# Optimization experiments

Measured on AMD Instinct MI355X. Metric: run time of the kernel, lower is better.

## Reference

```python
import jax, jax.numpy as jnp
import numpy as np
import math

D_MODEL = 512; NHEAD = 8; D_FF = 2048
DS_HEADS = 4; DS_DEPTH = 156; EPS = 1e-5
B = 128; N = 300; M = 300


def _ln(x, g, b):
    m = x.mean(-1, keepdims=True)
    v = ((x - m) ** 2).mean(-1, keepdims=True)
    return (x - m) / jnp.sqrt(v + EPS) * g + b


def _mish(x):
    return x * jnp.tanh(jax.nn.softplus(x))


def _mha(xq, xk, xv, in_w, in_b, out_w, out_b, nhead):
    D = xq.shape[-1]; dh = D // nhead
    wq, wk, wv = jnp.split(in_w, 3, axis=0)
    bq, bk, bv = jnp.split(in_b, 3)
    def proj(x, w, b):
        y = x @ w.T + b
        Bm, Nn, _ = y.shape
        return y.reshape(Bm, Nn, nhead, dh).transpose(0, 2, 1, 3)
    q, k, v = proj(xq, wq, bq), proj(xk, wk, bk), proj(xv, wv, bv)
    s = jnp.einsum('bhqd,bhkd->bhqk', q, k) / math.sqrt(dh)
    p = jax.nn.softmax(s, axis=-1)
    o = jnp.einsum('bhqk,bhkd->bhqd', p, v)
    Bm, _, Nn, _ = o.shape
    o = o.transpose(0, 2, 1, 3).reshape(Bm, Nn, D)
    return o @ out_w.T + out_b


def _custom_weight(p):
    # sequential kinematic-tree averaging on the post-softmax [...,24,24] matrix
    def upd(p, i, j, si, sj):
        return p.at[..., i, j].set((p[..., i, j] + p[..., si, sj]) * 0.5)
    p = upd(p, 0, 6, 0, 3); p = upd(p, 6, 0, 3, 0)
    p = upd(p, 0, 9, 0, 6); p = upd(p, 9, 0, 6, 0)
    for idx in (12, 13, 14):
        p = upd(p, 0, idx, 0, 9); p = upd(p, idx, 0, 9, 0)
    for s, tgt in ((13, 16), (14, 17), (12, 15)):
        p = upd(p, 0, tgt, 0, s); p = upd(p, tgt, 0, s, 0)
    return p


def _ds_attn(x, qk_w, v_w, lw, lb):
    Bm, Nn, _ = x.shape
    comb = jnp.einsum('bnf,fx->bnx', x, qk_w)
    q, k = jnp.split(comb, 2, axis=2)
    v = jnp.einsum('bnf,fx->bnx', x, v_w)
    def heads(y):
        return y.reshape(Bm, Nn, DS_HEADS, DS_DEPTH).transpose(0, 2, 1, 3)
    q, k, v = heads(q), heads(k), heads(v)  # [B,H,N,156]
    qs = q[..., 3:147].reshape(Bm, DS_HEADS, Nn, 24, 6)
    ks = k[..., 3:147].reshape(Bm, DS_HEADS, Nn, 24, 6)
    vs = v[..., 3:147].reshape(Bm, DS_HEADS, Nn, 24, 6)
    s = jnp.einsum('bhnij,bhnkj->bhnik', qs, ks) / math.sqrt(6.0)
    p = _custom_weight(jax.nn.softmax(s, axis=-1))
    o = jnp.einsum('bhnik,bhnkj->bhnij', p, vs).reshape(Bm, DS_HEADS, Nn, 144)
    v = v.at[..., 3:147].set(o)
    v = v.transpose(0, 2, 1, 3).reshape(Bm, Nn, DS_HEADS * DS_DEPTH)
    return v @ lw.T + lb


def _align(x_d, t, w, b):
    tt = t + x_d.mean(axis=-2)           # [B,D]
    h = _mish(tt) @ w.T + b              # [B,2D]
    weight, bias = jnp.split(h, 2, axis=-1)
    return (weight[:, None, :] + 1.0) * x_d + bias[:, None, :]


def _forward(tgt, memory, t, qk_w, v_w, ds_lw, ds_lb,
             ta_in_w, ta_in_b, ta_out_w, ta_out_b,
             ca_in_w, ca_in_b, ca_out_w, ca_out_b,
             l1_w, l1_b, l2_w, l2_b,
             n1_g, n1_b, n2_g, n2_b, n3_g, n3_b, n4_g, n4_b,
             a1_w, a1_b, a2_w, a2_b, a3_w, a3_b):
    x = tgt
    x = x + _ds_attn(_ln(x, n1_g, n1_b), qk_w, v_w, ds_lw, ds_lb)
    xn = _ln(x, n2_g, n2_b)
    x2 = _mha(xn, xn, xn, ta_in_w, ta_in_b, ta_out_w, ta_out_b, NHEAD)
    x = x + _align(x2, t, a1_w, a1_b)
    x3 = _mha(_ln(x, n3_g, n3_b), memory, memory, ca_in_w, ca_in_b, ca_out_w, ca_out_b, NHEAD)
    x = x + _align(x3, t, a2_w, a2_b)
    xn4 = _ln(x, n4_g, n4_b)
    x4 = jax.nn.relu(xn4 @ l1_w.T + l1_b) @ l2_w.T + l2_b
    x = x + _align(x4, t, a3_w, a3_b)
    return x


def setup_inputs():
    key = jax.random.key(0)
    ks = iter(jax.random.split(key, 64))
    def nrm(shape, s=0.02):
        return jax.random.normal(next(ks), shape, dtype=jnp.float32) * s
    z = lambda *shape: jnp.zeros(shape, jnp.float32)
    o = lambda *shape: jnp.ones(shape, jnp.float32)
    D = D_MODEL
    inp = {
        'tgt': jax.random.normal(next(ks), (B, N, D), dtype=jnp.float32),
        'memory': jax.random.normal(next(ks), (B, M, D), dtype=jnp.float32),
        't': jax.random.normal(next(ks), (B, D), dtype=jnp.float32),
        'qk_w': nrm((D, 2 * DS_DEPTH * DS_HEADS)),
        'v_w': nrm((D, DS_DEPTH * DS_HEADS)),
        'ds_lw': nrm((D, DS_DEPTH * DS_HEADS)), 'ds_lb': z(D),
        'ta_in_w': nrm((3 * D, D)), 'ta_in_b': z(3 * D),
        'ta_out_w': nrm((D, D)), 'ta_out_b': z(D),
        'ca_in_w': nrm((3 * D, D)), 'ca_in_b': z(3 * D),
        'ca_out_w': nrm((D, D)), 'ca_out_b': z(D),
        'l1_w': nrm((D_FF, D)), 'l1_b': z(D_FF),
        'l2_w': nrm((D, D_FF)), 'l2_b': z(D),
        'n1_g': o(D), 'n1_b': z(D), 'n2_g': o(D), 'n2_b': z(D),
        'n3_g': o(D), 'n3_b': z(D), 'n4_g': o(D), 'n4_b': z(D),
        'a1_w': nrm((2 * D, D)), 'a1_b': z(2 * D),
        'a2_w': nrm((2 * D, D)), 'a2_b': z(2 * D),
        'a3_w': nrm((2 * D, D)), 'a3_b': z(2 * D),
        'cond_drop_prob': 0,
    }
    return inp


def reference(tgt, memory, t, qk_w, v_w, ds_lw, ds_lb,
              ta_in_w, ta_in_b, ta_out_w, ta_out_b,
              ca_in_w, ca_in_b, ca_out_w, ca_out_b,
              l1_w, l1_b, l2_w, l2_b,
              n1_g, n1_b, n2_g, n2_b, n3_g, n3_b, n4_g, n4_b,
              a1_w, a1_b, a2_w, a2_b, a3_w, a3_b, cond_drop_prob):
    # cond_drop_prob is unused in the torch forward body (dropout eval mode)
    return _forward(tgt, memory, t, qk_w, v_w, ds_lw, ds_lb,
                    ta_in_w, ta_in_b, ta_out_w, ta_out_b,
                    ca_in_w, ca_in_b, ca_out_w, ca_out_b,
                    l1_w, l1_b, l2_w, l2_b,
                    n1_g, n1_b, n2_g, n2_b, n3_g, n3_b, n4_g, n4_b,
                    a1_w, a1_b, a2_w, a2_b, a3_w, a3_b)
```

## Files before the change

### kernel.cpp

```cpp
#include <hip/hip_runtime.h>
#include <math.h>

#define DEV __device__ __forceinline__

static constexpr int BB   = 128;
static constexpr int NN   = 300;
static constexpr int DM   = 512;

typedef __attribute__((ext_vector_type(8))) short short8;
typedef __attribute__((ext_vector_type(4))) float f32x4;

DEV unsigned short f2bf(float f) {
  unsigned u = __float_as_uint(f);
  unsigned r = (u + 0x7fffu + ((u >> 16) & 1u)) >> 16;
  return (unsigned short)r;
}
DEV float bf2f(unsigned short s) { return __uint_as_float((unsigned)s << 16); }
DEV unsigned pack_bf16x2(float a, float b) {
  return (unsigned)f2bf(a) | ((unsigned)f2bf(b) << 16);
}
DEV unsigned pack_trunc(float a, float b) {
  return (__float_as_uint(a) >> 16) | (__float_as_uint(b) & 0xffff0000u);
}

DEV void gld16(const void* g, void* l) {
  __builtin_amdgcn_global_load_lds(
      (const __attribute__((address_space(1))) unsigned int*)g,
      (__attribute__((address_space(3))) unsigned int*)l,
      16, 0, 0);
}

__global__ __launch_bounds__(256) void ln_kernel(
    const float* __restrict__ X, const float* __restrict__ g,
    const float* __restrict__ b, unsigned short* __restrict__ Y, int rows)
{
  int wv = threadIdx.x >> 6, lane = threadIdx.x & 63;
  int row = blockIdx.x * 4 + wv;
  if (row >= rows) return;
  const float* xp = X + (size_t)row * DM;
  float v[8]; float s = 0.f, s2 = 0.f;
#pragma unroll
  for (int j = 0; j < 8; j++) {
    v[j] = xp[lane + 64 * j]; s += v[j]; s2 += v[j] * v[j];
  }
#pragma unroll
  for (int o = 32; o >= 1; o >>= 1) { s += __shfl_xor(s, o); s2 += __shfl_xor(s2, o); }
  float mean = s * (1.f / 512.f);
  float var  = s2 * (1.f / 512.f) - mean * mean;
  float rstd = rsqrtf(var + 1e-5f);
  unsigned short* yp = Y + (size_t)row * DM;
#pragma unroll
  for (int j = 0; j < 8; j++) {
    int c = lane + 64 * j;
    yp[c] = f2bf((v[j] - mean) * rstd * g[c] + b[c]);
  }
}

__global__ __launch_bounds__(256) void align_ln(
    float* __restrict__ X, const float* __restrict__ Y,
    const float* __restrict__ H,
    const float* __restrict__ g, const float* __restrict__ bb,
    unsigned short* __restrict__ XN)
{
  int wv = threadIdx.x >> 6, lane = threadIdx.x & 63;
  int row = blockIdx.x * 4 + wv;
  int b = row / NN;
  float* xp = X + (size_t)row * DM;
  const float* yp = Y + (size_t)row * DM;
  const float* hw = H + (size_t)b * 1024;
  const float* hb = hw + 512;
  float v[8]; float s = 0.f, s2 = 0.f;
#pragma unroll
  for (int j = 0; j < 8; j++) {
    int c = lane + 64 * j;
    float xv = xp[c] + (hw[c] + 1.f) * yp[c] + hb[c];
    v[j] = xv; s += xv; s2 += xv * xv;
  }
#pragma unroll
  for (int j = 0; j < 8; j++) xp[lane + 64 * j] = v[j];
#pragma unroll
  for (int o = 32; o >= 1; o >>= 1) { s += __shfl_xor(s, o); s2 += __shfl_xor(s2, o); }
  float mean = s * (1.f / 512.f);
  float var  = s2 * (1.f / 512.f) - mean * mean;
  float rstd = rsqrtf(var + 1e-5f);
  unsigned short* yn = XN + (size_t)row * DM;
#pragma unroll
  for (int j = 0; j < 8; j++) {
    int c = lane + 64 * j;
    yn[c] = f2bf((v[j] - mean) * rstd * g[c] + bb[c]);
  }
}

__global__ __launch_bounds__(256) void cvt_bf16(
    const float* __restrict__ in, unsigned short* __restrict__ out, int n4)
{
  int i = blockIdx.x * 256 + threadIdx.x;
  if (i >= n4) return;
  float4 v = ((const float4*)in)[i];
  union { unsigned short s[4]; uint2 u; } o;
  o.s[0] = f2bf(v.x); o.s[1] = f2bf(v.y); o.s[2] = f2bf(v.z); o.s[3] = f2bf(v.w);
  *(uint2*)&out[(size_t)i * 4] = o.u;
}

__global__ __launch_bounds__(256) void cvt_pad_bf16(
    const float* __restrict__ in, unsigned short* __restrict__ out,
    int R, int C, int Cpad)
{
  int idx = blockIdx.x * 256 + threadIdx.x;
  int r = idx / Cpad, c = idx % Cpad;
  if (r >= R) return;
  out[idx] = (c < C) ? f2bf(in[(size_t)r * C + c]) : (unsigned short)0;
}

__global__ __launch_bounds__(256) void transpose_bf16(
    const float* __restrict__ in, unsigned short* __restrict__ out,
    int R, int Ccols, int Cpad)
{
  __shared__ float t[32][33];
  int c0 = blockIdx.x * 32, r0 = blockIdx.y * 32;
  int x = threadIdx.x & 31, y = threadIdx.x >> 5;
#pragma unroll
  for (int dy = 0; dy < 32; dy += 8) {
    int r = r0 + y + dy, c = c0 + x;
    t[y + dy][x] = (r < R && c < Ccols) ? in[(size_t)r * Ccols + c] : 0.f;
  }
  __syncthreads();
#pragma unroll
  for (int dy = 0; dy < 32; dy += 8) {
    int c = c0 + y + dy, r = r0 + x;
    if (c < Cpad && r < R) out[(size_t)c * R + r] = f2bf(t[x][y + dy]);
  }
}

template<int EPI>
__global__ __launch_bounds__(256) void gemm_bb(
    const unsigned short* __restrict__ A, int lda,
    const unsigned short* __restrict__ W, int ldw,
    const float* __restrict__ bias,
    const float* __restrict__ R, int ldr,
    void* __restrict__ Cv, int ldc,
    int M, int K, int NC)
{
  __shared__ __align__(16) unsigned short As[128 * 32];
  __shared__ __align__(16) unsigned short Bs[128 * 32];
  const int tid = threadIdx.x;
  const int wave = tid >> 6, lane = tid & 63;
  const int wr = wave >> 1, wc = wave & 1;
  const int quad = lane >> 4, l16 = lane & 15;

  const unsigned nx = gridDim.x, nwg = nx * gridDim.y;
  const unsigned orig = blockIdx.y * nx + blockIdx.x;
  const unsigned qq = nwg >> 3, rr = nwg & 7;
  const unsigned xcd = orig & 7, idx = orig >> 3;
  const unsigned swz = (xcd < rr) ? (xcd * (qq + 1) + idx)
                                  : (rr * (qq + 1) + (xcd - rr) * qq + idx);
  const int n0 = (int)(swz % nx) * 128;
  const int m0 = (int)(swz / nx) * 128;

  int ra = m0 + (tid >> 2);
  int ra0 = (ra      >= M) ? M - 1 : ra;
  int ra1 = (ra + 64 >= M) ? M - 1 : ra + 64;
  const unsigned short* a0 = A + (size_t)ra0 * lda + (tid & 3) * 8;
  const unsigned short* a1 = A + (size_t)ra1 * lda + (tid & 3) * 8;
  const unsigned short* b0 = W + (size_t)(n0 + (tid >> 2)) * ldw + (tid & 3) * 8;
  const unsigned short* b1 = b0 + (size_t)64 * ldw;
  unsigned short* dA0 = &As[wave * 512];
  unsigned short* dA1 = &As[2048 + wave * 512];
  unsigned short* dB0 = &Bs[wave * 512];
  unsigned short* dB1 = &Bs[2048 + wave * 512];

  f32x4 acc[4][4];
#pragma unroll
  for (int i = 0; i < 4; i++)
#pragma unroll
    for (int j = 0; j < 4; j++) acc[i][j] = (f32x4){0.f, 0.f, 0.f, 0.f};

  for (int k0 = 0; k0 < K; k0 += 32) {
    gld16(a0 + k0, dA0);
    gld16(a1 + k0, dA1);
    gld16(b0 + k0, dB0);
    gld16(b1 + k0, dB1);
    __syncthreads();
    short8 af[4], bq[4];
#pragma unroll
    for (int i = 0; i < 4; i++)
      af[i] = *(const short8*)&As[(wr * 64 + i * 16 + l16) * 32 + quad * 8];
#pragma unroll
    for (int j = 0; j < 4; j++)
      bq[j] = *(const short8*)&Bs[(wc * 64 + j * 16 + l16) * 32 + quad * 8];
#pragma unroll
    for (int i = 0; i < 4; i++)
#pragma unroll
      for (int j = 0; j < 4; j++)
        acc[i][j] = __builtin_amdgcn_mfma_f32_16x16x32_bf16(af[i], bq[j], acc[i][j], 0, 0, 0);
    __syncthreads();
  }

#pragma unroll
  for (int i = 0; i < 4; i++) {
    int rbase = m0 + wr * 64 + i * 16 + quad * 4;
#pragma unroll
    for (int r = 0; r < 4; r++) {
      int row = rbase + r;
      if (row < M) {
        size_t rowc = (size_t)row * ldc;
#pragma unroll
        for (int j = 0; j < 4; j++) {
          int col = n0 + wc * 64 + j * 16 + l16;
          if (col < NC) {
            float e = acc[i][j][r];
            if (EPI == 1 || EPI == 2 || EPI == 3 || EPI == 5) e += bias[col];
            if (EPI == 3) e += R[(size_t)row * ldr + col];
            if (EPI == 2) {
              ((unsigned short*)Cv)[rowc + col] = f2bf(fmaxf(e, 0.f));
            } else if (EPI == 5 || EPI == 6) {
              ((unsigned short*)Cv)[rowc + col] = f2bf(e);
            } else {
              ((float*)Cv)[rowc + col] = e;
            }
          }
        }
      }
    }
  }
}

__global__ __launch_bounds__(256) void ds_attn_kernel(
    const float* __restrict__ COMB, unsigned short* __restrict__ V)
{
  __shared__ float ks[4][2][24][6];
  __shared__ float vs[4][2][24][6];
  int wv = threadIdx.x >> 6, lane = threadIdx.x & 63;
  int half = lane >> 5, i = lane & 31;
  int u  = blockIdx.x * 4 + wv;
  int bn = u >> 1, hp = u & 1;
  int h  = hp * 2 + half;
  size_t cbase = (size_t)bn * 1248 + h * 156 + 3;
  size_t vbase = (size_t)bn * 640  + h * 156 + 3;

  float q[6];
  if (i < 24) {
#pragma unroll
    for (int j = 0; j < 6; j++) {
      q[j]                 = COMB[cbase + i * 6 + j];
      ks[wv][half][i][j]   = COMB[cbase + 624 + i * 6 + j];
      vs[wv][half][i][j]   = bf2f(V[vbase + i * 6 + j]);
    }
  } else {
#pragma unroll
    for (int j = 0; j < 6; j++) q[j] = 0.f;
  }
  __syncthreads();

  float p[24];
#pragma unroll
  for (int k = 0; k < 24; k++) p[k] = 0.f;

  if (i < 24) {
    float mx = -1e30f;
#pragma unroll
    for (int k = 0; k < 24; k++) {
      float s = 0.f;
#pragma unroll
      for (int j = 0; j < 6; j++) s += q[j] * ks[wv][half][k][j];
      s *= 0.4082482904638631f;
      p[k] = s; mx = fmaxf(mx, s);
    }
    float sum = 0.f;
#pragma unroll
    for (int k = 0; k < 24; k++) { p[k] = __expf(p[k] - mx); sum += p[k]; }
    float inv = 1.f / sum;
#pragma unroll
    for (int k = 0; k < 24; k++) p[k] *= inv;
  }

  {
    float c = p[0];
    float t;
    t = __shfl(c, 3, 32);  if (i == 6) c = (c + t) * 0.5f;
    t = __shfl(c, 6, 32);  if (i == 9) c = (c + t) * 0.5f;
    t = __shfl(c, 9, 32);  if (i >= 12 && i <= 14) c = (c + t) * 0.5f;
    int src = (i >= 3) ? (i - 3) : 0;
    t = __shfl(c, src, 32); if (i >= 15 && i <= 17) c = (c + t) * 0.5f;
    p[0] = c;
  }
  if (i == 0) {
    p[6]  = (p[6]  + p[3])  * 0.5f;
    p[9]  = (p[9]  + p[6])  * 0.5f;
    p[12] = (p[12] + p[9])  * 0.5f;
    p[13] = (p[13] + p[9])  * 0.5f;
    p[14] = (p[14] + p[9])  * 0.5f;
    p[16] = (p[16] + p[13]) * 0.5f;
    p[17] = (p[17] + p[14]) * 0.5f;
    p[15] = (p[15] + p[12]) * 0.5f;
  }

  if (i < 24) {
    float o[6] = {0.f, 0.f, 0.f, 0.f, 0.f, 0.f};
#pragma unroll
    for (int k = 0; k < 24; k++) {
#pragma unroll
      for (int j = 0; j < 6; j++) o[j] += p[k] * vs[wv][half][k][j];
    }
#pragma unroll
    for (int j = 0; j < 6; j++) V[vbase + i * 6 + j] = f2bf(o[j]);
  }
}

__global__ __launch_bounds__(512) void mha_mfma(
    const unsigned short* __restrict__ Qp, int ldq, int qoff,
    const unsigned short* __restrict__ KVp, int ldkv, int koff, int voff,
    unsigned short* __restrict__ Op, float scale)
{
  __shared__ __align__(16) unsigned short Ksh[304 * 72];
  __shared__ __align__(16) unsigned short Qsh[304 * 72];
  __shared__ __align__(16) unsigned short Vt[64 * 328];
  __shared__ __align__(16) unsigned short Pt[8][16 * 68];
  const int bh = blockIdx.x, b = bh >> 3, h = bh & 7;
  const int tid = threadIdx.x, wv = tid >> 6, lane = tid & 63;
  const int quad = lane >> 4, l16 = lane & 15;
  const size_t kbase = (size_t)b * NN * ldkv + koff + h * 64;
  const size_t vbase = (size_t)b * NN * ldkv + voff + h * 64;
  const size_t qbase = (size_t)b * NN * ldq  + qoff + h * 64;

  for (int f = tid; f < 304 * 8; f += 512) {
    int rk = f >> 3, c8 = (f & 7) * 8;
    short8 wk, wq;
    if (rk < 300) {
      wk = *(const short8*)(KVp + kbase + (size_t)rk * ldkv + c8);
      wq = *(const short8*)(Qp  + qbase + (size_t)rk * ldq  + c8);
    } else {
      union { uint4 u; short8 s; } z; z.u = make_uint4(0u, 0u, 0u, 0u);
      wk = z.s; wq = z.s;
    }
    *(short8*)&Ksh[rk * 72 + c8] = wk;
    *(short8*)&Qsh[rk * 72 + c8] = wq;
  }
  for (int f = tid; f < 64 * 164; f += 512) {
    int d = f & 63, s0 = (f >> 6) * 2;
    unsigned w = 0u;
    if (s0 < 300) {
      unsigned short v0 = KVp[vbase + (size_t)s0 * ldkv + d];
      unsigned short v1 = (s0 + 1 < 300) ? KVp[vbase + (size_t)(s0 + 1) * ldkv + d]
                                         : (unsigned short)0;
      w = (unsigned)v0 | ((unsigned)v1 << 16);
    }
    *(unsigned*)&Vt[d * 328 + s0] = w;
  }
  __syncthreads();

  unsigned short* pt = &Pt[wv][0];

  for (int qt = wv; qt < 19; qt += 8) {
    int qr = qt * 16 + l16;
    short8 qf[2];
    qf[0] = *(const short8*)&Qsh[qr * 72 + quad * 8];
    qf[1] = *(const short8*)&Qsh[qr * 72 + 32 + quad * 8];

    f32x4 sacc[19];
#pragma unroll
    for (int t = 0; t < 19; t++) {
      short8 k0 = *(const short8*)&Ksh[(t * 16 + l16) * 72 + quad * 8];
      short8 k1 = *(const short8*)&Ksh[(t * 16 + l16) * 72 + 32 + quad * 8];
      f32x4 a = (f32x4){0.f, 0.f, 0.f, 0.f};
      a = __builtin_amdgcn_mfma_f32_16x16x32_bf16(k0, qf[0], a, 0, 0, 0);
      a = __builtin_amdgcn_mfma_f32_16x16x32_bf16(k1, qf[1], a, 0, 0, 0);
      sacc[t] = a;
    }

    float mx = -1e30f;
#pragma unroll
    for (int t = 0; t < 19; t++)
#pragma unroll
      for (int r = 0; r < 4; r++) mx = fmaxf(mx, sacc[t][r]);
    mx = fmaxf(mx, __shfl_xor(mx, 16));
    mx = fmaxf(mx, __shfl_xor(mx, 32));
    float sum = 0.f;
#pragma unroll
    for (int t = 0; t < 19; t++) {
#pragma unroll
      for (int r = 0; r < 4; r++) {
        float p = __expf((sacc[t][r] - mx) * scale);
        if (t == 18 && quad == 3) p = 0.f;
        sacc[t][r] = p; sum += p;
      }
    }
    sum += __shfl_xor(sum, 16);
    sum += __shfl_xor(sum, 32);
    float inv = 1.f / sum;

    f32x4 oacc[4];
#pragma unroll
    for (int dt = 0; dt < 4; dt++) oacc[dt] = (f32x4){0.f, 0.f, 0.f, 0.f};
#pragma unroll
    for (int c = 0; c < 10; c++) {
#pragma unroll
      for (int tic = 0; tic < 2; tic++) {
        int t = 2 * c + tic;
        unsigned w0 = 0u, w1 = 0u;
        if (t < 19) {
          w0 = pack_trunc(sacc[t][0], sacc[t][1]);
          w1 = pack_trunc(sacc[t][2], sacc[t][3]);
        }
        *(unsigned*)&pt[l16 * 68 + tic * 16 + quad * 4]     = w0;
        *(unsigned*)&pt[l16 * 68 + tic * 16 + quad * 4 + 2] = w1;
      }
      short8 pa = *(const short8*)&pt[l16 * 68 + quad * 8];
#pragma unroll
      for (int dt = 0; dt < 4; dt++) {
        short8 vb = *(const short8*)&Vt[(dt * 16 + l16) * 328 + c * 32 + quad * 8];
        oacc[dt] = __builtin_amdgcn_mfma_f32_16x16x32_bf16(pa, vb, oacc[dt], 0, 0, 0);
      }
    }

#pragma unroll
    for (int r = 0; r < 4; r++) {
      float iv = __shfl(inv, quad * 4 + r);
#pragma unroll
      for (int dt = 0; dt < 4; dt++)
        pt[(quad * 4 + r) * 68 + dt * 16 + l16] = f2bf(oacc[dt][r] * iv);
    }
#pragma unroll
    for (int rep = 0; rep < 2; rep++) {
      int idx = rep * 64 + lane;
      int rl = idx >> 3, seg = idx & 7;
      int row = qt * 16 + rl;
      uint4 w = *(const uint4*)&pt[rl * 68 + seg * 8];
      if (row < 300)
        *(uint4*)(Op + (size_t)(b * NN + row) * DM + h * 64 + seg * 8) = w;
    }
  }
}

__global__ __launch_bounds__(256) void colmean_mish(
    const float* __restrict__ Y, const float* __restrict__ tvec,
    unsigned short* __restrict__ mm)
{
  int g = blockIdx.x * 256 + threadIdx.x;
  int b = g >> 9, d = g & 511;
  const float* yp = Y + (size_t)b * NN * DM + d;
  float s = 0.f;
  for (int n = 0; n < NN; n++) s += yp[(size_t)n * DM];
  float v = tvec[g] + s * (1.f / 300.f);
  float sp = (v > 20.f) ? v : log1pf(__expf(v));
  mm[g] = f2bf(v * tanhf(sp));
}

__global__ __launch_bounds__(256) void align_apply(
    float* __restrict__ X, const float* __restrict__ Y,
    const float* __restrict__ H)
{
  int idx = blockIdx.x * 256 + threadIdx.x;
  int row = idx >> 7;
  int d4  = (idx & 127) * 4;
  int b   = row / NN;
  float4 y = *(const float4*)&Y[(size_t)row * DM + d4];
  float4 x = *(const float4*)&X[(size_t)row * DM + d4];
  const float* hw = H + (size_t)b * 1024 + d4;
  const float* hb = hw + 512;
  x.x += (hw[0] + 1.f) * y.x + hb[0];
  x.y += (hw[1] + 1.f) * y.y + hb[1];
  x.z += (hw[2] + 1.f) * y.z + hb[2];
  x.w += (hw[3] + 1.f) * y.w + hb[3];
  *(float4*)&X[(size_t)row * DM + d4] = x;
}

extern "C" void kernel_launch(void* const* d_in, const int* in_sizes, int n_in,
                              void* d_out, int out_size, void* d_ws, size_t ws_size,
                              hipStream_t stream)
{
  const float* tgt      = (const float*)d_in[0];
  const float* memory   = (const float*)d_in[1];
  const float* tvec     = (const float*)d_in[2];
  const float* qk_w     = (const float*)d_in[3];
  const float* v_w      = (const float*)d_in[4];
  const float* ds_lw    = (const float*)d_in[5];
  const float* ds_lb    = (const float*)d_in[6];
  const float* ta_in_w  = (const float*)d_in[7];
  const float* ta_in_b  = (const float*)d_in[8];
  const float* ta_out_w = (const float*)d_in[9];
  const float* ta_out_b = (const float*)d_in[10];
  const float* ca_in_w  = (const float*)d_in[11];
  const float* ca_in_b  = (const float*)d_in[12];
  const float* ca_out_w = (const float*)d_in[13];
  const float* ca_out_b = (const float*)d_in[14];
  const float* l1_w     = (const float*)d_in[15];
  const float* l1_b     = (const float*)d_in[16];
  const float* l2_w     = (const float*)d_in[17];
  const float* l2_b     = (const float*)d_in[18];
  const float* n1_g = (const float*)d_in[19]; const float* n1_b = (const float*)d_in[20];
  const float* n2_g = (const float*)d_in[21]; const float* n2_b = (const float*)d_in[22];
  const float* n3_g = (const float*)d_in[23]; const float* n3_b = (const float*)d_in[24];
  const float* n4_g = (const float*)d_in[25]; const float* n4_b = (const float*)d_in[26];
  const float* a1_w = (const float*)d_in[27]; const float* a1_b = (const float*)d_in[28];
  const float* a2_w = (const float*)d_in[29]; const float* a2_b = (const float*)d_in[30];
  const float* a3_w = (const float*)d_in[31]; const float* a3_b = (const float*)d_in[32];

  const size_t W_QKT = 1280ULL * 512 * 2;
  const size_t W_VT  = 640ULL  * 512 * 2;
  const size_t W_TAI = 1536ULL * 512 * 2;
  const size_t W_TAO = 512ULL  * 512 * 2;
  const size_t W_CAI = 1536ULL * 512 * 2;
  const size_t W_CAO = 512ULL  * 512 * 2;
  const size_t W_L1  = 2048ULL * 512 * 2;
  const size_t W_L2  = 512ULL  * 2048 * 2;
  const size_t W_DSL = 512ULL  * 640 * 2;
  const size_t W_AX  = 1024ULL * 512 * 2;
  const size_t W_MEM = (size_t)BB * NN * 512 * 2;
  const size_t fixedB = W_QKT + W_VT + W_TAI + W_TAO + W_CAI + W_CAO
                      + W_L1 + W_L2 + W_DSL + 3 * W_AX + W_MEM;
  const size_t per_b = 300ULL * (1024 + 4992 + 1280 + 2048) + 1024 + 4096;
  int Bc = 128;
  while (Bc > 16 && fixedB + (size_t)Bc * per_b > ws_size) Bc >>= 1;
  const int rows = Bc * NN;
  const int mB   = (rows + 127) / 128;
  const int aB   = (Bc + 127) / 128;
  const int nchunks = BB / Bc;

  char* p = (char*)d_ws;
  unsigned short* qkTh  = (unsigned short*)p; p += W_QKT;
  unsigned short* vTh   = (unsigned short*)p; p += W_VT;
  unsigned short* taiWh = (unsigned short*)p; p += W_TAI;
  unsigned short* taoWh = (unsigned short*)p; p += W_TAO;
  unsigned short* caiWh = (unsigned short*)p; p += W_CAI;
  unsigned short* caoWh = (unsigned short*)p; p += W_CAO;
  unsigned short* l1Wh  = (unsigned short*)p; p += W_L1;
  unsigned short* l2Wh  = (unsigned short*)p; p += W_L2;
  unsigned short* dslWh = (unsigned short*)p; p += W_DSL;
  unsigned short* a1Wh  = (unsigned short*)p; p += W_AX;
  unsigned short* a2Wh  = (unsigned short*)p; p += W_AX;
  unsigned short* a3Wh  = (unsigned short*)p; p += W_AX;
  unsigned short* memh  = (unsigned short*)p; p += W_MEM;
  unsigned short* XNh   = (unsigned short*)p; p += (size_t)rows * 512 * 2;
  char* SCRB = p;                             p += (size_t)rows * 4992;
  unsigned short* Vdsh  = (unsigned short*)p; p += (size_t)rows * 640 * 2;
  float* Yb  = (float*)p; p += (size_t)rows * 512 * 4;
  unsigned short* MMh = (unsigned short*)p;   p += (size_t)Bc * 512 * 2;
  float* Hb  = (float*)p;

  float* COMB = (float*)SCRB;
  unsigned short* QKVh = (unsigned short*)SCRB;
  unsigned short* T2h  = (unsigned short*)SCRB;

  dim3 thr(256);

  transpose_bf16<<<dim3(40, 16), thr, 0, stream>>>(qk_w, qkTh, 512, 1248, 1280);
  transpose_bf16<<<dim3(20, 16), thr, 0, stream>>>(v_w,  vTh,  512, 624, 640);
  cvt_pad_bf16<<<dim3(512 * 640 / 256), thr, 0, stream>>>(ds_lw, dslWh, 512, 624, 640);
  auto cvt = [&](const float* src, unsigned short* dst, size_t n) {
    int n4 = (int)(n / 4);
    cvt_bf16<<<dim3((n4 + 255) / 256), thr, 0, stream>>>(src, dst, n4);
  };
  cvt(ta_in_w,  taiWh, 1536ULL * 512);
  cvt(ta_out_w, taoWh, 512ULL * 512);
  cvt(ca_in_w,  caiWh, 1536ULL * 512);
  cvt(ca_out_w, caoWh, 512ULL * 512);
  cvt(l1_w,     l1Wh,  2048ULL * 512);
  cvt(l2_w,     l2Wh,  512ULL * 2048);
  cvt(a1_w,     a1Wh,  1024ULL * 512);
  cvt(a2_w,     a2Wh,  1024ULL * 512);
  cvt(a3_w,     a3Wh,  1024ULL * 512);
  cvt(memory,   memh,  (size_t)BB * NN * 512);

  for (int c = 0; c < nchunks; ++c) {
    const size_t roff = (size_t)c * Bc * NN * DM;
    const float* tgtC = tgt    + roff;
    const float* tC   = tvec   + (size_t)c * Bc * 512;
    const unsigned short* memhC = memh + roff;
    float*       XC   = (float*)d_out + roff;

    ln_kernel<<<rows / 4, thr, 0, stream>>>(tgtC, n1_g, n1_b, XNh, rows);
    gemm_bb<0><<<dim3(10, mB), thr, 0, stream>>>(XNh, 512, qkTh, 512, nullptr, nullptr, 0, COMB, 1248, rows, 512, 1248);
    gemm_bb<6><<<dim3(5, mB),  thr, 0, stream>>>(XNh, 512, vTh,  512, nullptr, nullptr, 0, Vdsh, 640,  rows, 512, 640);
    ds_attn_kernel<<<rows / 2, thr, 0, stream>>>(COMB, Vdsh);
    gemm_bb<3><<<dim3(4, mB),  thr, 0, stream>>>(Vdsh, 640, dslWh, 640, ds_lb, tgtC, 512, XC, 512, rows, 640, 512);

    ln_kernel<<<rows / 4, thr, 0, stream>>>(XC, n2_g, n2_b, XNh, rows);
    gemm_bb<5><<<dim3(12, mB), thr, 0, stream>>>(XNh, 512, taiWh, 512, ta_in_b, nullptr, 0, QKVh, 1536, rows, 512, 1536);
    mha_mfma<<<Bc * 8, 512, 0, stream>>>(QKVh, 1536, 0, QKVh, 1536, 512, 1024, XNh, 0.125f);
    gemm_bb<1><<<dim3(4, mB),  thr, 0, stream>>>(XNh, 512, taoWh, 512, ta_out_b, nullptr, 0, Yb, 512, rows, 512, 512);
    colmean_mish<<<Bc * 2, thr, 0, stream>>>(Yb, tC, MMh);
    gemm_bb<1><<<dim3(8, aB),  thr, 0, stream>>>(MMh, 512, a1Wh, 512, a1_b, nullptr, 0, Hb, 1024, Bc, 512, 1024);
    align_ln<<<rows / 4, thr, 0, stream>>>(XC, Yb, Hb, n3_g, n3_b, XNh);

    gemm_bb<5><<<dim3(4, mB),  thr, 0, stream>>>(XNh, 512, caiWh, 512, ca_in_b, nullptr, 0, QKVh, 1536, rows, 512, 512);
    gemm_bb<5><<<dim3(8, mB),  thr, 0, stream>>>(memhC, 512, caiWh + 512 * 512, 512, ca_in_b + 512, nullptr, 0, QKVh + 512, 1536, rows, 512, 1024);
    mha_mfma<<<Bc * 8, 512, 0, stream>>>(QKVh, 1536, 0, QKVh, 1536, 512, 1024, XNh, 0.125f);
    gemm_bb<1><<<dim3(4, mB),  thr, 0, stream>>>(XNh, 512, caoWh, 512, ca_out_b, nullptr, 0, Yb, 512, rows, 512, 512);
    colmean_mish<<<Bc * 2, thr, 0, stream>>>(Yb, tC, MMh);
    gemm_bb<1><<<dim3(8, aB),  thr, 0, stream>>>(MMh, 512, a2Wh, 512, a2_b, nullptr, 0, Hb, 1024, Bc, 512, 1024);
    align_ln<<<rows / 4, thr, 0, stream>>>(XC, Yb, Hb, n4_g, n4_b, XNh);

    gemm_bb<2><<<dim3(16, mB), thr, 0, stream>>>(XNh, 512, l1Wh, 512, l1_b, nullptr, 0, T2h, 2048, rows, 512, 2048);
    gemm_bb<1><<<dim3(4, mB),  thr, 0, stream>>>(T2h, 2048, l2Wh, 2048, l2_b, nullptr, 0, Yb, 512, rows, 2048, 512);
    colmean_mish<<<Bc * 2, thr, 0, stream>>>(Yb, tC, MMh);
    gemm_bb<1><<<dim3(8, aB),  thr, 0, stream>>>(MMh, 512, a3Wh, 512, a3_b, nullptr, 0, Hb, 1024, Bc, 512, 1024);
    align_apply<<<rows / 2, thr, 0, stream>>>(XC, Yb, Hb);
  }
}
```

Baseline: 2.295 ms.

## Write QKV in head-major layout, fuse DS qk/v GEMMs, store COMB as bf16

The QKV projection GEMMs now scatter their output into a head-major [sec][head][row][64] bf16 layout. mha_mfma can then load K, V and Q contiguously, and it reads Q fragments straight from global memory instead of staging them in shared memory. The depth-split qk and v projections are merged into one GEMM over a concatenated weight, and the COMB intermediate is stored in bf16 instead of fp32, which shrinks scratch and memory traffic. The trade-offs are scattered epilogue stores, lower precision on q/k, and uncoalesced global Q reads.

```diff
diff --git a/kernel.cpp b/kernel.cpp
--- a/kernel.cpp
+++ b/kernel.cpp
@@ -16,9 +16,6 @@
   return (unsigned short)r;
 }
 DEV float bf2f(unsigned short s) { return __uint_as_float((unsigned)s << 16); }
-DEV unsigned pack_bf16x2(float a, float b) {
-  return (unsigned)f2bf(a) | ((unsigned)f2bf(b) << 16);
-}
 DEV unsigned pack_trunc(float a, float b) {
   return (__float_as_uint(a) >> 16) | (__float_as_uint(b) & 0xffff0000u);
 }
@@ -139,7 +136,7 @@
     const float* __restrict__ bias,
     const float* __restrict__ R, int ldr,
     void* __restrict__ Cv, int ldc,
-    int M, int K, int NC)
+    int M, int K, int NC, int coloff)
 {
   __shared__ __align__(16) unsigned short As[128 * 32];
   __shared__ __align__(16) unsigned short Bs[128 * 32];
@@ -209,12 +206,19 @@
           int col = n0 + wc * 64 + j * 16 + l16;
           if (col < NC) {
             float e = acc[i][j][r];
-            if (EPI == 1 || EPI == 2 || EPI == 3 || EPI == 5) e += bias[col];
+            if (EPI == 1 || EPI == 2 || EPI == 3 || EPI == 7) e += bias[col];
             if (EPI == 3) e += R[(size_t)row * ldr + col];
             if (EPI == 2) {
               ((unsigned short*)Cv)[rowc + col] = f2bf(fmaxf(e, 0.f));
-            } else if (EPI == 5 || EPI == 6) {
-              ((unsigned short*)Cv)[rowc + col] = f2bf(e);
+            } else if (EPI == 7) {
+              int cc = col + coloff;
+              int sec = cc >> 9, hh = (cc >> 6) & 7, dh = cc & 63;
+              ((unsigned short*)Cv)[(((size_t)(sec * 8 + hh)) * M + row) * 64 + dh] = f2bf(e);
+            } else if (EPI == 8) {
+              if (col < 1248)
+                ((unsigned short*)Cv)[(size_t)row * 1248 + col] = f2bf(e);
+              else if (col >= 1280)
+                ((unsigned short*)(void*)R)[(size_t)row * 640 + (col - 1280)] = f2bf(e);
             } else {
               ((float*)Cv)[rowc + col] = e;
             }
@@ -226,7 +230,7 @@
 }
 
 __global__ __launch_bounds__(256) void ds_attn_kernel(
-    const float* __restrict__ COMB, unsigned short* __restrict__ V)
+    const unsigned short* __restrict__ COMB, unsigned short* __restrict__ V)
 {
   __shared__ float ks[4][2][24][6];
   __shared__ float vs[4][2][24][6];
@@ -242,8 +246,8 @@
   if (i < 24) {
 #pragma unroll
     for (int j = 0; j < 6; j++) {
-      q[j]                 = COMB[cbase + i * 6 + j];
-      ks[wv][half][i][j]   = COMB[cbase + 624 + i * 6 + j];
+      q[j]                 = bf2f(COMB[cbase + i * 6 + j]);
+      ks[wv][half][i][j]   = bf2f(COMB[cbase + 624 + i * 6 + j]);
       vs[wv][half][i][j]   = bf2f(V[vbase + i * 6 + j]);
     }
   } else {
@@ -308,41 +312,35 @@
 }
 
 __global__ __launch_bounds__(512) void mha_mfma(
-    const unsigned short* __restrict__ Qp, int ldq, int qoff,
-    const unsigned short* __restrict__ KVp, int ldkv, int koff, int voff,
-    unsigned short* __restrict__ Op, float scale)
+    const unsigned short* __restrict__ QKV3, unsigned short* __restrict__ Op,
+    int rowsT, float scale)
 {
   __shared__ __align__(16) unsigned short Ksh[304 * 72];
-  __shared__ __align__(16) unsigned short Qsh[304 * 72];
   __shared__ __align__(16) unsigned short Vt[64 * 328];
   __shared__ __align__(16) unsigned short Pt[8][16 * 68];
   const int bh = blockIdx.x, b = bh >> 3, h = bh & 7;
   const int tid = threadIdx.x, wv = tid >> 6, lane = tid & 63;
   const int quad = lane >> 4, l16 = lane & 15;
-  const size_t kbase = (size_t)b * NN * ldkv + koff + h * 64;
-  const size_t vbase = (size_t)b * NN * ldkv + voff + h * 64;
-  const size_t qbase = (size_t)b * NN * ldq  + qoff + h * 64;
+  const unsigned short* Qp = QKV3 + ((size_t)h        * rowsT + b * NN) * 64;
+  const unsigned short* Kp = QKV3 + ((size_t)(8 + h)  * rowsT + b * NN) * 64;
+  const unsigned short* Vp = QKV3 + ((size_t)(16 + h) * rowsT + b * NN) * 64;
 
   for (int f = tid; f < 304 * 8; f += 512) {
     int rk = f >> 3, c8 = (f & 7) * 8;
-    short8 wk, wq;
+    short8 w;
     if (rk < 300) {
-      wk = *(const short8*)(KVp + kbase + (size_t)rk * ldkv + c8);
-      wq = *(const short8*)(Qp  + qbase + (size_t)rk * ldq  + c8);
+      w = *(const short8*)(Kp + f * 8);
     } else {
-      union { uint4 u; short8 s; } z; z.u = make_uint4(0u, 0u, 0u, 0u);
-      wk = z.s; wq = z.s;
-    }
-    *(short8*)&Ksh[rk * 72 + c8] = wk;
-    *(short8*)&Qsh[rk * 72 + c8] = wq;
+      union { uint4 u; short8 s; } z; z.u = make_uint4(0u, 0u, 0u, 0u); w = z.s;
+    }
+    *(short8*)&Ksh[rk * 72 + c8] = w;
   }
   for (int f = tid; f < 64 * 164; f += 512) {
     int d = f & 63, s0 = (f >> 6) * 2;
     unsigned w = 0u;
     if (s0 < 300) {
-      unsigned short v0 = KVp[vbase + (size_t)s0 * ldkv + d];
-      unsigned short v1 = (s0 + 1 < 300) ? KVp[vbase + (size_t)(s0 + 1) * ldkv + d]
-                                         : (unsigned short)0;
+      unsigned short v0 = Vp[s0 * 64 + d];
+      unsigned short v1 = (s0 + 1 < 300) ? Vp[(s0 + 1) * 64 + d] : (unsigned short)0;
       w = (unsigned)v0 | ((unsigned)v1 << 16);
     }
     *(unsigned*)&Vt[d * 328 + s0] = w;
@@ -352,10 +350,10 @@
   unsigned short* pt = &Pt[wv][0];
 
   for (int qt = wv; qt < 19; qt += 8) {
-    int qr = qt * 16 + l16;
+    int qr = qt * 16 + l16; if (qr > 299) qr = 299;
     short8 qf[2];
-    qf[0] = *(const short8*)&Qsh[qr * 72 + quad * 8];
-    qf[1] = *(const short8*)&Qsh[qr * 72 + 32 + quad * 8];
+    qf[0] = *(const short8*)(Qp + qr * 64 + quad * 8);
+    qf[1] = *(const short8*)(Qp + qr * 64 + 32 + quad * 8);
 
     f32x4 sacc[19];
 #pragma unroll
@@ -496,8 +494,7 @@
   const float* a2_w = (const float*)d_in[29]; const float* a2_b = (const float*)d_in[30];
   const float* a3_w = (const float*)d_in[31]; const float* a3_b = (const float*)d_in[32];
 
-  const size_t W_QKT = 1280ULL * 512 * 2;
-  const size_t W_VT  = 640ULL  * 512 * 2;
+  const size_t W_W2  = 1920ULL * 512 * 2;
   const size_t W_TAI = 1536ULL * 512 * 2;
   const size_t W_TAO = 512ULL  * 512 * 2;
   const size_t W_CAI = 1536ULL * 512 * 2;
@@ -507,9 +504,9 @@
   const size_t W_DSL = 512ULL  * 640 * 2;
   const size_t W_AX  = 1024ULL * 512 * 2;
   const size_t W_MEM = (size_t)BB * NN * 512 * 2;
-  const size_t fixedB = W_QKT + W_VT + W_TAI + W_TAO + W_CAI + W_CAO
+  const size_t fixedB = W_W2 + W_TAI + W_TAO + W_CAI + W_CAO
                       + W_L1 + W_L2 + W_DSL + 3 * W_AX + W_MEM;
-  const size_t per_b = 300ULL * (1024 + 4992 + 1280 + 2048) + 1024 + 4096;
+  const size_t per_b = 300ULL * (1024 + 4096 + 1280 + 2048) + 1024 + 4096;
   int Bc = 128;
   while (Bc > 16 && fixedB + (size_t)Bc * per_b > ws_size) Bc >>= 1;
   const int rows = Bc * NN;
@@ -518,8 +515,7 @@
   const int nchunks = BB / Bc;
 
   char* p = (char*)d_ws;
-  unsigned short* qkTh  = (unsigned short*)p; p += W_QKT;
-  unsigned short* vTh   = (unsigned short*)p; p += W_VT;
+  unsigned short* W2h   = (unsigned short*)p; p += W_W2;
   unsigned short* taiWh = (unsigned short*)p; p += W_TAI;
   unsigned short* taoWh = (unsigned short*)p; p += W_TAO;
   unsigned short* caiWh = (unsigned short*)p; p += W_CAI;
@@ -532,20 +528,20 @@
   unsigned short* a3Wh  = (unsigned short*)p; p += W_AX;
   unsigned short* memh  = (unsigned short*)p; p += W_MEM;
   unsigned short* XNh   = (unsigned short*)p; p += (size_t)rows * 512 * 2;
-  char* SCRB = p;                             p += (size_t)rows * 4992;
+  char* SCRB = p;                             p += (size_t)rows * 4096;
   unsigned short* Vdsh  = (unsigned short*)p; p += (size_t)rows * 640 * 2;
   float* Yb  = (float*)p; p += (size_t)rows * 512 * 4;
   unsigned short* MMh = (unsigned short*)p;   p += (size_t)Bc * 512 * 2;
   float* Hb  = (float*)p;
 
-  float* COMB = (float*)SCRB;
-  unsigned short* QKVh = (unsigned short*)SCRB;
-  unsigned short* T2h  = (unsigned short*)SCRB;
+  unsigned short* COMBh = (unsigned short*)SCRB;
+  unsigned short* QKV3  = (unsigned short*)SCRB;
+  unsigned short* T2h   = (unsigned short*)SCRB;
 
   dim3 thr(256);
 
-  transpose_bf16<<<dim3(40, 16), thr, 0, stream>>>(qk_w, qkTh, 512, 1248, 1280);
-  transpose_bf16<<<dim3(20, 16), thr, 0, stream>>>(v_w,  vTh,  512, 624, 640);
+  transpose_bf16<<<dim3(40, 16), thr, 0, stream>>>(qk_w, W2h, 512, 1248, 1280);
+  transpose_bf16<<<dim3(20, 16), thr, 0, stream>>>(v_w,  W2h + 1280 * 512, 512, 624, 640);
   cvt_pad_bf16<<<dim3(512 * 640 / 256), thr, 0, stream>>>(ds_lw, dslWh, 512, 624, 640);
   auto cvt = [&](const float* src, unsigned short* dst, size_t n) {
     int n4 = (int)(n / 4);
@@ -570,31 +566,30 @@
     float*       XC   = (float*)d_out + roff;
 
     ln_kernel<<<rows / 4, thr, 0, stream>>>(tgtC, n1_g, n1_b, XNh, rows);
-    gemm_bb<0><<<dim3(10, mB), thr, 0, stream>>>(XNh, 512, qkTh, 512, nullptr, nullptr, 0, COMB, 1248, rows, 512, 1248);
-    gemm_bb<6><<<dim3(5, mB),  thr, 0, stream>>>(XNh, 512, vTh,  512, nullptr, nullptr, 0, Vdsh, 640,  rows, 512, 640);
-    ds_attn_kernel<<<rows / 2, thr, 0, stream>>>(COMB, Vdsh);
-    gemm_bb<3><<<dim3(4, mB),  thr, 0, stream>>>(Vdsh, 640, dslWh, 640, ds_lb, tgtC, 512, XC, 512, rows, 640, 512);
+    gemm_bb<8><<<dim3(15, mB), thr, 0, stream>>>(XNh, 512, W2h, 512, nullptr, (const float*)Vdsh, 0, COMBh, 1248, rows, 512, 1920, 0);
+    ds_attn_kernel<<<rows / 2, thr, 0, stream>>>(COMBh, Vdsh);
+    gemm_bb<3><<<dim3(4, mB),  thr, 0, stream>>>(Vdsh, 640, dslWh, 640, ds_lb, tgtC, 512, XC, 512, rows, 640, 512, 0);
 
     ln_kernel<<<rows / 4, thr, 0, stream>>>(XC, n2_g, n2_b, XNh, rows);
-    gemm_bb<5><<<dim3(12, mB), thr, 0, stream>>>(XNh, 512, taiWh, 512, ta_in_b, nullptr, 0, QKVh, 1536, rows, 512, 1536);
-    mha_mfma<<<Bc * 8, 512, 0, stream>>>(QKVh, 1536, 0, QKVh, 1536, 512, 1024, XNh, 0.125f);
-    gemm_bb<1><<<dim3(4, mB),  thr, 0, stream>>>(XNh, 512, taoWh, 512, ta_out_b, nullptr, 0, Yb, 512, rows, 512, 512);
+    gemm_bb<7><<<dim3(12, mB), thr, 0, stream>>>(XNh, 512, taiWh, 512, ta_in_b, nullptr, 0, QKV3, 0, rows, 512, 1536, 0);
+    mha_mfma<<<Bc * 8, 512, 0, stream>>>(QKV3, XNh, rows, 0.125f);
+    gemm_bb<1><<<dim3(4, mB),  thr, 0, stream>>>(XNh, 512, taoWh, 512, ta_out_b, nullptr, 0, Yb, 512, rows, 512, 512, 0);
     colmean_mish<<<Bc * 2, thr, 0, stream>>>(Yb, tC, MMh);
-    gemm_bb<1><<<dim3(8, aB),  thr, 0, stream>>>(MMh, 512, a1Wh, 512, a1_b, nullptr, 0, Hb, 1024, Bc, 512, 1024);
+    gemm_bb<1><<<dim3(8, aB),  thr, 0, stream>>>(MMh, 512, a1Wh, 512, a1_b, nullptr, 0, Hb, 1024, Bc, 512, 1024, 0);
     align_ln<<<rows / 4, thr, 0, stream>>>(XC, Yb, Hb, n3_g, n3_b, XNh);
 
-    gemm_bb<5><<<dim3(4, mB),  thr, 0, stream>>>(XNh, 512, caiWh, 512, ca_in_b, nullptr, 0, QKVh, 1536, rows, 512, 512);
-    gemm_bb<5><<<dim3(8, mB),  thr, 0, stream>>>(memhC, 512, caiWh + 512 * 512, 512, ca_in_b + 512, nullptr, 0, QKVh + 512, 1536, rows, 512, 1024);
-    mha_mfma<<<Bc * 8, 512, 0, stream>>>(QKVh, 1536, 0, QKVh, 1536, 512, 1024, XNh, 0.125f);
-    gemm_bb<1><<<dim3(4, mB),  thr, 0, stream>>>(XNh, 512, caoWh, 512, ca_out_b, nullptr, 0, Yb, 512, rows, 512, 512);
+    gemm_bb<7><<<dim3(4, mB),  thr, 0, stream>>>(XNh, 512, caiWh, 512, ca_in_b, nullptr, 0, QKV3, 0, rows, 512, 512, 0);
+    gemm_bb<7><<<dim3(8, mB),  thr, 0, stream>>>(memhC, 512, caiWh + 512 * 512, 512, ca_in_b + 512, nullptr, 0, QKV3, 0, rows, 512, 1024, 512);
+    mha_mfma<<<Bc * 8, 512, 0, stream>>>(QKV3, XNh, rows, 0.125f);
+    gemm_bb<1><<<dim3(4, mB),  thr, 0, stream>>>(XNh, 512, caoWh, 512, ca_out_b, nullptr, 0, Yb, 512, rows, 512, 512, 0);
     colmean_mish<<<Bc * 2, thr, 0, stream>>>(Yb, tC, MMh);
-    gemm_bb<1><<<dim3(8, aB),  thr, 0, stream>>>(MMh, 512, a2Wh, 512, a2_b, nullptr, 0, Hb, 1024, Bc, 512, 1024);
+    gemm_bb<1><<<dim3(8, aB),  thr, 0, stream>>>(MMh, 512, a2Wh, 512, a2_b, nullptr, 0, Hb, 1024, Bc, 512, 1024, 0);
     align_ln<<<rows / 4, thr, 0, stream>>>(XC, Yb, Hb, n4_g, n4_b, XNh);
 
-    gemm_bb<2><<<dim3(16, mB), thr, 0, stream>>>(XNh, 512, l1Wh, 512, l1_b, nullptr, 0, T2h, 2048, rows, 512, 2048);
-    gemm_bb<1><<<dim3(4, mB),  thr, 0, stream>>>(T2h, 2048, l2Wh, 2048, l2_b, nullptr, 0, Yb, 512, rows, 2048, 512);
+    gemm_bb<2><<<dim3(16, mB), thr, 0, stream>>>(XNh, 512, l1Wh, 512, l1_b, nullptr, 0, T2h, 2048, rows, 512, 2048, 0);
+    gemm_bb<1><<<dim3(4, mB),  thr, 0, stream>>>(T2h, 2048, l2Wh, 2048, l2_b, nullptr, 0, Yb, 512, rows, 2048, 512, 0);
     colmean_mish<<<Bc * 2, thr, 0, stream>>>(Yb, tC, MMh);
-    gemm_bb<1><<<dim3(8, aB),  thr, 0, stream>>>(MMh, 512, a3Wh, 512, a3_b, nullptr, 0, Hb, 1024, Bc, 512, 1024);
+    gemm_bb<1><<<dim3(8, aB),  thr, 0, stream>>>(MMh, 512, a3Wh, 512, a3_b, nullptr, 0, Hb, 1024, Bc, 512, 1024, 0);
     align_apply<<<rows / 2, thr, 0, stream>>>(XC, Yb, Hb);
   }
 }
```

Measured after the change: 2.340 ms. No clear change (+2.0%).
